# Performance work log

Hardware: AMD Instinct MI355X
Metric: run time of the kernel (lower is better)

## Reference

```python
import jax, jax.numpy as jnp
import numpy as np

# Sizes: batch=32, in_channels=32, out_channels=64, grid 256x256, modes1=modes2=32
B, CI, CO, NX, NY, M1, M2 = 32, 32, 64, 256, 256, 32, 32


def setup_inputs() -> dict:
    key = jax.random.key(0)
    k1, k2, k3 = jax.random.split(key, 3)
    scale = 1.0 / (CI * CO)
    return {
        "x": jax.random.normal(k1, (B, CI, NX, NY), dtype=jnp.float32),
        "w_real": scale * jax.random.uniform(k2, (CI, CO, 2 * M1, M2 + 1), dtype=jnp.float32),
        "w_imag": scale * jax.random.uniform(k3, (CI, CO, 2 * M1, M2 + 1), dtype=jnp.float32),
        "modes1": M1,
        "modes2": M2,
    }


def reference(x, w_real, w_imag, modes1, modes2):
    # rfft2 with 'forward' normalization (divide by nx*ny), as in torch.fft.rfft2(norm='forward')
    xf = jnp.fft.rfft2(x, norm="forward")  # (b, i, nx, ny//2+1) complex64
    # resize_rfft2(xf, (2*modes1, 2*modes2)) in the truncation regime (nx >= 2*m1, ny//2+1 >= m2+1):
    # keep first modes2+1 columns (rfft axis) and the first/last modes1 rows (full fft axis).
    xt = jnp.concatenate(
        [xf[..., :modes1, : modes2 + 1], xf[..., -modes1:, : modes2 + 1]], axis=-2
    )  # (b, i, 2*m1, m2+1)
    W = w_real + 1j * w_imag  # (i, o, 2*m1, m2+1) complex
    # complex channel mixing, keep only real part
    y = jnp.einsum("bixy,ioxy->boxy", xt, W).real  # (b, o, 2*m1, m2+1)
    # signed mode-sum: double-count conjugate-symmetric modes, correct the (0,0) DC mode
    out = (
        2.0 * jnp.sum(y[..., :modes1, :], axis=(-2, -1))
        + 2.0 * jnp.sum(y[..., modes1:, 1:], axis=(-2, -1))
        - y[..., 0, 0]
    )  # (b, o)
    return out
```

## Files before the change

kernel.cpp:

```cpp
#include <hip/hip_runtime.h>
#include <math.h>

#define BATCH 32
#define CIn   32
#define COut  64

typedef __attribute__((ext_vector_type(8))) short bf16x8;
typedef __attribute__((ext_vector_type(4))) float f32x4;

#define OB_T1F  0u
#define OB_ECF  40960u
#define OB_ESF  73728u
#define OB_XTB  106496u
#define OB_PART 8757248u

__device__ __forceinline__ ushort f2bf(float f) {
    union { float f; uint u; } v; v.f = f;
    uint r = (v.u + 0x7FFFu + ((v.u >> 16) & 1u)) >> 16;
    return (ushort)r;
}

__device__ __forceinline__ bf16x8 cvt8(f32x4 lo, f32x4 hi) {
    bf16x8 r;
    r[0] = (short)f2bf(lo[0]); r[1] = (short)f2bf(lo[1]);
    r[2] = (short)f2bf(lo[2]); r[3] = (short)f2bf(lo[3]);
    r[4] = (short)f2bf(hi[0]); r[5] = (short)f2bf(hi[1]);
    r[6] = (short)f2bf(hi[2]); r[7] = (short)f2bf(hi[3]);
    return r;
}

#define NB0 0
#define NB1 16
#define NB2 32
#define NB3 48
#define NB4 50

__global__ void fno_tw(ushort* __restrict__ T1f, ushort* __restrict__ Ecf,
                       ushort* __restrict__ Esf) {
    const int nb[5] = {NB0, NB1, NB2, NB3, NB4};
    int idx = blockIdx.x * 256 + threadIdx.x;
    const float w0 = 6.28318530717958647692f / 256.0f;
    if (idx < 20480) {
        int i = idx & 7, l = (idx >> 3) & 63, ct = idx >> 9;
        int c = ct / 5, t = ct - 5 * c;
        int k = 32 * c + 8 * (l >> 4) + i;
        int n = nb[t] + (l & 15);
        int ky = n >> 1, s = n & 1;
        int m = (k * ky) & 255;
        float v = s ? -sinf(w0 * (float)m) : cosf(w0 * (float)m);
        T1f[idx] = f2bf(v * (1.0f / 65536.0f));
    }
    if (idx < 16384) {
        int i = idx & 7, l = (idx >> 3) & 63, km = idx >> 9;
        int ks = km >> 2, mt = km & 3;
        int xx = ks * 32 + ((l >> 4) << 3) + i;
        int kx = mt * 16 + (l & 15);
        int kxa = (kx < 32) ? kx : kx + 192;
        int m = (xx * kxa) & 255;
        Ecf[idx] = f2bf(cosf(w0 * (float)m));
        Esf[idx] = f2bf(-sinf(w0 * (float)m));
    }
}

#define MFMA5(CG, AV)                                                              \
    acc0 = __builtin_amdgcn_mfma_f32_16x16x32_bf16((AV), bfr[(CG)*5+0], acc0, 0,0,0); \
    acc1 = __builtin_amdgcn_mfma_f32_16x16x32_bf16((AV), bfr[(CG)*5+1], acc1, 0,0,0); \
    acc2 = __builtin_amdgcn_mfma_f32_16x16x32_bf16((AV), bfr[(CG)*5+2], acc2, 0,0,0); \
    acc3 = __builtin_amdgcn_mfma_f32_16x16x32_bf16((AV), bfr[(CG)*5+3], acc3, 0,0,0); \
    acc4 = __builtin_amdgcn_mfma_f32_16x16x32_bf16((AV), bfr[(CG)*5+4], acc4, 0,0,0);

#define STAGE_CG(CG) do {                                                          \
    int cg_ = (CG);                                                                \
    const float* base_ = x + ((size_t)p * 256 + (size_t)(cg_ >> 2) * 64) * 256     \
                           + (cg_ & 3) * 64;                                       \
    float* buf_ = &smx[cg_ & 1][0];                                                \
    _Pragma("unroll")                                                              \
    for (int j = 0; j < 4; ++j) {                                                  \
        int rr_ = ((w * 4 + j) << 2) + (lane >> 4);                                \
        int sg_ = (lane & 15) ^ (rr_ & 7);                                         \
        const float* gp_ = base_ + (size_t)rr_ * 256 + (sg_ << 2);                 \
        char* lp_ = (char*)buf_ + ((w * 4 + j) << 10);                             \
        __builtin_amdgcn_global_load_lds(                                          \
            (const __attribute__((address_space(1))) unsigned int*)gp_,            \
            (__attribute__((address_space(3))) unsigned int*)lp_, 16, 0, 0);       \
    } } while (0)

#define WAITV(N) do {                                                              \
    asm volatile("s_waitcnt vmcnt(" #N ")" ::: "memory");                          \
    __builtin_amdgcn_sched_barrier(0); } while (0)

#define WAITL0 do {                                                                \
    asm volatile("s_waitcnt lgkmcnt(0)" ::: "memory");                             \
    __builtin_amdgcn_sched_barrier(0); } while (0)

#define YTW(ACC, T) do {                                                           \
    int n_ = nb[T] + r0;                                                           \
    if ((T) != 4 || r0 >= 14) {                                                    \
        _Pragma("unroll")                                                          \
        for (int j = 0; j < 4; ++j) {                                              \
            int xrow_ = sl * 64 + w * 16 + 4 * g + j;                              \
            int us_ = n_ * 256 + ((((xrow_ >> 3) ^ (n_ & 31)) << 3) | (xrow_ & 7));\
            Yt[us_] = f2bf((ACC)[j]);                                              \
        } } } while (0)

__global__ __launch_bounds__(256, 2)
void fno_fused(const float* __restrict__ x, const ushort* __restrict__ T1f,
               const ushort* __restrict__ Ecf, const ushort* __restrict__ Esf,
               ushort* __restrict__ XTb) {
    __shared__ float smx[2][4096];
    __shared__ __align__(16) ushort Yt[16896];
    const int nb[5] = {NB0, NB1, NB2, NB3, NB4};
    const int tid  = threadIdx.x;
    const int lane = tid & 63;
    const int w    = tid >> 6;
    const int r0   = lane & 15;
    const int g    = lane >> 4;
    const int p    = blockIdx.x;

    bf16x8 bfr[40];
    const bf16x8* bp = (const bf16x8*)T1f;
#pragma unroll
    for (int q = 0; q < 40; ++q) bfr[q] = bp[q * 64 + lane];

    const int rr = (w << 4) + r0;
    const int xr = rr & 7;

    STAGE_CG(0);
    STAGE_CG(1);

    f32x4 acc0, acc1, acc2, acc3, acc4;
#pragma unroll
    for (int cg = 0; cg < 16; ++cg) {
        if ((cg & 3) == 0) {
            acc0 = (f32x4){0,0,0,0}; acc1 = (f32x4){0,0,0,0};
            acc2 = (f32x4){0,0,0,0}; acc3 = (f32x4){0,0,0,0};
            acc4 = (f32x4){0,0,0,0};
        }
        if (cg < 15) { WAITV(4); } else { WAITV(0); }

        const float* rowp = &smx[cg & 1][rr * 64];
        f32x4 lo0 = *(const f32x4*)&rowp[(((g << 1)    ) ^ xr) << 2];
        f32x4 hi0 = *(const f32x4*)&rowp[(((g << 1) + 1) ^ xr) << 2];
        f32x4 lo1 = *(const f32x4*)&rowp[((8 + (g << 1)    ) ^ xr) << 2];
        f32x4 hi1 = *(const f32x4*)&rowp[((8 + (g << 1) + 1) ^ xr) << 2];
        WAITL0;
        if (cg + 2 < 16) STAGE_CG(cg + 2);

        bf16x8 a0v = cvt8(lo0, hi0);
        bf16x8 a1v = cvt8(lo1, hi1);
        MFMA5(2 * (cg & 3)    , a0v);
        MFMA5(2 * (cg & 3) + 1, a1v);

        if ((cg & 3) == 3) {
            int sl = cg >> 2;
            YTW(acc0, 0); YTW(acc1, 1); YTW(acc2, 2); YTW(acc3, 3); YTW(acc4, 4);
        }
    }
    __syncthreads();

    const int mt = w;
    f32x4 P1[5], P2[5];
#pragma unroll
    for (int t = 0; t < 5; ++t) { P1[t] = (f32x4){0,0,0,0}; P2[t] = (f32x4){0,0,0,0}; }

    const bf16x8* ecp = (const bf16x8*)Ecf;
    const bf16x8* esp = (const bf16x8*)Esf;
#pragma unroll
    for (int ks = 0; ks < 8; ++ks) {
        bf16x8 ea = ecp[(ks * 4 + mt) * 64 + lane];
        bf16x8 es = esp[(ks * 4 + mt) * 64 + lane];
#pragma unroll
        for (int t = 0; t < 5; ++t) {
            int n = nb[t] + r0;
            bf16x8 b = *(const bf16x8*)&Yt[n * 256 + ((((ks << 2) + g) ^ (n & 31)) << 3)];
            P1[t] = __builtin_amdgcn_mfma_f32_16x16x32_bf16(ea, b, P1[t], 0, 0, 0);
            P2[t] = __builtin_amdgcn_mfma_f32_16x16x32_bf16(es, b, P2[t], 0, 0, 0);
        }
    }

    ushort* xtl = (ushort*)&smx[0][0];
#pragma unroll
    for (int t = 0; t < 5; ++t) {
        int n  = nb[t] + r0;
        int ky = n >> 1, im = n & 1;
#pragma unroll
        for (int j = 0; j < 4; ++j) {
            float v2x = __shfl_xor(P2[t][j], 1);
            if (t == 4 && r0 < 14) continue;
            int kx = mt * 16 + 4 * g + j;
            float val = im ? (P1[t][j] + v2x) : (P1[t][j] - v2x);
            float wgt = (kx < 32) ? ((kx == 0 && ky == 0) ? 1.f : 2.f)
                                  : ((ky == 0) ? 0.f : 2.f);
            if (im) wgt = -wgt;
            xtl[kx * 66 + n] = f2bf(wgt * val);
        }
    }
    __syncthreads();

    const uint4* srcq = (const uint4*)xtl;
    uint4* dstq = (uint4*)(XTb + (size_t)p * 4224);
    for (int e = tid; e < 528; e += 256) dstq[e] = srcq[e];
}

__global__ __launch_bounds__(256)
void fno_gemm3(const ushort* __restrict__ XTb, const float* __restrict__ Wr,
               const float* __restrict__ Wi, float* __restrict__ part) {
    const int blk = blockIdx.x;
    const int ic  = blk / 22;
    const int sc  = blk - ic * 22;
    const int tid = threadIdx.x;
    const int lane = tid & 63;
    const int w    = tid >> 6;
    const int r0   = lane & 15;
    const int g    = lane >> 4;
    const int o    = (w << 4) + r0;

    const float* wrp = Wr + ((size_t)ic * 64 + o) * 2112 + sc * 96 + 4 * g;
    const float* wip = Wi + ((size_t)ic * 64 + o) * 2112 + sc * 96 + 4 * g;
    const ushort* a0 = XTb + ((size_t)r0 * 32 + ic) * 4224 + sc * 192 + 8 * g;
    const ushort* a1 = a0 + (size_t)16 * 32 * 4224;

    f32x4 acc0 = {0,0,0,0}, acc1 = {0,0,0,0};
#pragma unroll
    for (int st = 0; st < 6; ++st) {
        f32x4 vr = *(const f32x4*)(wrp + st * 16);
        f32x4 vi = *(const f32x4*)(wip + st * 16);
        bf16x8 b;
        b[0] = (short)f2bf(vr[0]); b[1] = (short)f2bf(vi[0]);
        b[2] = (short)f2bf(vr[1]); b[3] = (short)f2bf(vi[1]);
        b[4] = (short)f2bf(vr[2]); b[5] = (short)f2bf(vi[2]);
        b[6] = (short)f2bf(vr[3]); b[7] = (short)f2bf(vi[3]);
        bf16x8 af0 = *(const bf16x8*)(a0 + st * 32);
        bf16x8 af1 = *(const bf16x8*)(a1 + st * 32);
        acc0 = __builtin_amdgcn_mfma_f32_16x16x32_bf16(af0, b, acc0, 0, 0, 0);
        acc1 = __builtin_amdgcn_mfma_f32_16x16x32_bf16(af1, b, acc1, 0, 0, 0);
    }

    float* pp = part + (size_t)blk * 2048;
#pragma unroll
    for (int j = 0; j < 4; ++j) {
        pp[(4 * g + j) * 64 + o]      = acc0[j];
        pp[(16 + 4 * g + j) * 64 + o] = acc1[j];
    }
}

__global__ __launch_bounds__(256)
void fno_reduce(const float* __restrict__ part, float* __restrict__ out) {
    __shared__ float red[8][32];
    const int tid = threadIdx.x;
    const int il  = tid & 31;
    const int js  = tid >> 5;
    const int idx = blockIdx.x * 32 + il;

    float s = 0.f;
#pragma unroll 4
    for (int t = 0; t < 88; ++t)
        s += part[(size_t)(js + 8 * t) * 2048 + idx];
    red[js][il] = s;
    __syncthreads();

    if (tid < 32) {
        float v = red[0][tid] + red[1][tid] + red[2][tid] + red[3][tid]
                + red[4][tid] + red[5][tid] + red[6][tid] + red[7][tid];
        out[blockIdx.x * 32 + tid] = v;
    }
}

extern "C" void kernel_launch(void* const* d_in, const int* in_sizes, int n_in,
                              void* d_out, int out_size, void* d_ws, size_t ws_size,
                              hipStream_t stream) {
    const float* x  = (const float*)d_in[0];
    const float* wr = (const float*)d_in[1];
    const float* wi = (const float*)d_in[2];
    float* out = (float*)d_out;
    char* ws   = (char*)d_ws;

    ushort* T1f = (ushort*)(ws + OB_T1F);
    ushort* Ecf = (ushort*)(ws + OB_ECF);
    ushort* Esf = (ushort*)(ws + OB_ESF);
    ushort* XTb = (ushort*)(ws + OB_XTB);
    float* part = (float*)(ws + OB_PART);

    fno_tw<<<80, 256, 0, stream>>>(T1f, Ecf, Esf);
    fno_fused<<<1024, 256, 0, stream>>>(x, T1f, Ecf, Esf, XTb);
    fno_gemm3<<<704, 256, 0, stream>>>(XTb, wr, wi, part);
    fno_reduce<<<64, 256, 0, stream>>>(part, out);
}
```

Before: 85.03 us.

## Deepen x staging pipeline, use packed bf16 conversion, widen reduce grid

The fused DFT kernel now stages x in smaller 32-column chunks through a four-deep LDS ring, with three loads in flight. It prefetches the next chunk's LDS reads into registers before issuing the current MFMAs, so global latency and LDS reads overlap with matrix work. Scalar float-to-bf16 rounding is replaced with the HIP packed __float22bfloat162_rn conversions across all kernels, which cuts ALU work. The final reduction runs on 256 blocks instead of 64 to raise parallelism. The cost is more vmcnt bookkeeping and more loop iterations, each with smaller per-iteration work.

```diff
diff --git a/kernel.cpp b/kernel.cpp
--- a/kernel.cpp
+++ b/kernel.cpp
@@ -1,4 +1,5 @@
 #include <hip/hip_runtime.h>
+#include <hip/hip_bf16.h>
 #include <math.h>
 
 #define BATCH 32
@@ -20,13 +21,18 @@
     return (ushort)r;
 }
 
+__device__ __forceinline__ ushort f2bfn(float f) {
+    union { __hip_bfloat16 h; ushort u; } v;
+    v.h = __float2bfloat16(f);
+    return v.u;
+}
 __device__ __forceinline__ bf16x8 cvt8(f32x4 lo, f32x4 hi) {
-    bf16x8 r;
-    r[0] = (short)f2bf(lo[0]); r[1] = (short)f2bf(lo[1]);
-    r[2] = (short)f2bf(lo[2]); r[3] = (short)f2bf(lo[3]);
-    r[4] = (short)f2bf(hi[0]); r[5] = (short)f2bf(hi[1]);
-    r[6] = (short)f2bf(hi[2]); r[7] = (short)f2bf(hi[3]);
-    return r;
+    union { __hip_bfloat162 h2[4]; bf16x8 v; } u;
+    u.h2[0] = __float22bfloat162_rn(make_float2(lo[0], lo[1]));
+    u.h2[1] = __float22bfloat162_rn(make_float2(lo[2], lo[3]));
+    u.h2[2] = __float22bfloat162_rn(make_float2(hi[0], hi[1]));
+    u.h2[3] = __float22bfloat162_rn(make_float2(hi[2], hi[3]));
+    return u.v;
 }
 
 #define NB0 0
@@ -62,28 +68,33 @@
     }
 }
 
-#define MFMA5(CG, AV)                                                              \
-    acc0 = __builtin_amdgcn_mfma_f32_16x16x32_bf16((AV), bfr[(CG)*5+0], acc0, 0,0,0); \
-    acc1 = __builtin_amdgcn_mfma_f32_16x16x32_bf16((AV), bfr[(CG)*5+1], acc1, 0,0,0); \
-    acc2 = __builtin_amdgcn_mfma_f32_16x16x32_bf16((AV), bfr[(CG)*5+2], acc2, 0,0,0); \
-    acc3 = __builtin_amdgcn_mfma_f32_16x16x32_bf16((AV), bfr[(CG)*5+3], acc3, 0,0,0); \
-    acc4 = __builtin_amdgcn_mfma_f32_16x16x32_bf16((AV), bfr[(CG)*5+4], acc4, 0,0,0);
+#define MFMA5(KC, AV)                                                              \
+    acc0 = __builtin_amdgcn_mfma_f32_16x16x32_bf16((AV), bfr[(KC)*5+0], acc0, 0,0,0); \
+    acc1 = __builtin_amdgcn_mfma_f32_16x16x32_bf16((AV), bfr[(KC)*5+1], acc1, 0,0,0); \
+    acc2 = __builtin_amdgcn_mfma_f32_16x16x32_bf16((AV), bfr[(KC)*5+2], acc2, 0,0,0); \
+    acc3 = __builtin_amdgcn_mfma_f32_16x16x32_bf16((AV), bfr[(KC)*5+3], acc3, 0,0,0); \
+    acc4 = __builtin_amdgcn_mfma_f32_16x16x32_bf16((AV), bfr[(KC)*5+4], acc4, 0,0,0);
 
 #define STAGE_CG(CG) do {                                                          \
     int cg_ = (CG);                                                                \
-    const float* base_ = x + ((size_t)p * 256 + (size_t)(cg_ >> 2) * 64) * 256     \
-                           + (cg_ & 3) * 64;                                       \
-    float* buf_ = &smx[cg_ & 1][0];                                                \
+    int sl_ = cg_ >> 3, kc_ = cg_ & 7;                                             \
     _Pragma("unroll")                                                              \
-    for (int j = 0; j < 4; ++j) {                                                  \
-        int rr_ = ((w * 4 + j) << 2) + (lane >> 4);                                \
-        int sg_ = (lane & 15) ^ (rr_ & 7);                                         \
-        const float* gp_ = base_ + (size_t)rr_ * 256 + (sg_ << 2);                 \
-        char* lp_ = (char*)buf_ + ((w * 4 + j) << 10);                             \
+    for (int j = 0; j < 2; ++j) {                                                  \
+        int rws_ = 8 * j + (lane >> 3);                                            \
+        int sg_  = (lane & 7) ^ (rws_ & 7);                                        \
+        const float* gp_ = x + ((size_t)p * 256 + sl_ * 64 + w * 16 + rws_) * 256  \
+                             + kc_ * 32 + (sg_ << 2);                              \
+        char* lp_ = (char*)&smx[cg_ & 3][0] + w * 2048 + j * 1024 + (lane << 4);   \
         __builtin_amdgcn_global_load_lds(                                          \
             (const __attribute__((address_space(1))) unsigned int*)gp_,            \
             (__attribute__((address_space(3))) unsigned int*)lp_, 16, 0, 0);       \
     } } while (0)
+
+#define DSR(CG, RA, RB) do {                                                       \
+    const char* base_ = (const char*)&smx[(CG) & 3][0] + w * 2048 + r0 * 128;      \
+    (RA) = *(const f32x4*)(base_ + ((((g << 1)    ) ^ xr) << 4));                  \
+    (RB) = *(const f32x4*)(base_ + ((((g << 1) + 1) ^ xr) << 4));                  \
+    } while (0)
 
 #define WAITV(N) do {                                                              \
     asm volatile("s_waitcnt vmcnt(" #N ")" ::: "memory");                          \
@@ -100,14 +111,14 @@
         for (int j = 0; j < 4; ++j) {                                              \
             int xrow_ = sl * 64 + w * 16 + 4 * g + j;                              \
             int us_ = n_ * 256 + ((((xrow_ >> 3) ^ (n_ & 31)) << 3) | (xrow_ & 7));\
-            Yt[us_] = f2bf((ACC)[j]);                                              \
+            Yt[us_] = f2bfn((ACC)[j]);                                             \
         } } } while (0)
 
 __global__ __launch_bounds__(256, 2)
 void fno_fused(const float* __restrict__ x, const ushort* __restrict__ T1f,
                const ushort* __restrict__ Ecf, const ushort* __restrict__ Esf,
                ushort* __restrict__ XTb) {
-    __shared__ float smx[2][4096];
+    __shared__ float smx[4][2048];
     __shared__ __align__(16) ushort Yt[16896];
     const int nb[5] = {NB0, NB1, NB2, NB3, NB4};
     const int tid  = threadIdx.x;
@@ -115,6 +126,7 @@
     const int w    = tid >> 6;
     const int r0   = lane & 15;
     const int g    = lane >> 4;
+    const int xr   = r0 & 7;
     const int p    = blockIdx.x;
 
     bf16x8 bfr[40];
@@ -122,37 +134,30 @@
 #pragma unroll
     for (int q = 0; q < 40; ++q) bfr[q] = bp[q * 64 + lane];
 
-    const int rr = (w << 4) + r0;
-    const int xr = rr & 7;
-
-    STAGE_CG(0);
-    STAGE_CG(1);
+    f32x4 rA[2][2];
+
+    STAGE_CG(0); STAGE_CG(1); STAGE_CG(2);
+    WAITV(4);
+    DSR(0, rA[0][0], rA[0][1]);
 
     f32x4 acc0, acc1, acc2, acc3, acc4;
 #pragma unroll
-    for (int cg = 0; cg < 16; ++cg) {
-        if ((cg & 3) == 0) {
+    for (int cg = 0; cg < 32; ++cg) {
+        if ((cg & 7) == 0) {
             acc0 = (f32x4){0,0,0,0}; acc1 = (f32x4){0,0,0,0};
             acc2 = (f32x4){0,0,0,0}; acc3 = (f32x4){0,0,0,0};
             acc4 = (f32x4){0,0,0,0};
         }
-        if (cg < 15) { WAITV(4); } else { WAITV(0); }
-
-        const float* rowp = &smx[cg & 1][rr * 64];
-        f32x4 lo0 = *(const f32x4*)&rowp[(((g << 1)    ) ^ xr) << 2];
-        f32x4 hi0 = *(const f32x4*)&rowp[(((g << 1) + 1) ^ xr) << 2];
-        f32x4 lo1 = *(const f32x4*)&rowp[((8 + (g << 1)    ) ^ xr) << 2];
-        f32x4 hi1 = *(const f32x4*)&rowp[((8 + (g << 1) + 1) ^ xr) << 2];
         WAITL0;
-        if (cg + 2 < 16) STAGE_CG(cg + 2);
-
-        bf16x8 a0v = cvt8(lo0, hi0);
-        bf16x8 a1v = cvt8(lo1, hi1);
-        MFMA5(2 * (cg & 3)    , a0v);
-        MFMA5(2 * (cg & 3) + 1, a1v);
-
-        if ((cg & 3) == 3) {
-            int sl = cg >> 2;
+        bf16x8 af = cvt8(rA[cg & 1][0], rA[cg & 1][1]);
+        if (cg + 3 < 32) STAGE_CG(cg + 3);
+        if (cg <= 28)      { WAITV(4); }
+        else if (cg == 29) { WAITV(2); }
+        else if (cg == 30) { WAITV(0); }
+        if (cg + 1 < 32) DSR(cg + 1, rA[(cg + 1) & 1][0], rA[(cg + 1) & 1][1]);
+        MFMA5(cg & 7, af);
+        if ((cg & 7) == 7) {
+            int sl = cg >> 3;
             YTW(acc0, 0); YTW(acc1, 1); YTW(acc2, 2); YTW(acc3, 3); YTW(acc4, 4);
         }
     }
@@ -192,7 +197,7 @@
             float wgt = (kx < 32) ? ((kx == 0 && ky == 0) ? 1.f : 2.f)
                                   : ((ky == 0) ? 0.f : 2.f);
             if (im) wgt = -wgt;
-            xtl[kx * 66 + n] = f2bf(wgt * val);
+            xtl[kx * 66 + n] = f2bfn(wgt * val);
         }
     }
     __syncthreads();
@@ -225,15 +230,15 @@
     for (int st = 0; st < 6; ++st) {
         f32x4 vr = *(const f32x4*)(wrp + st * 16);
         f32x4 vi = *(const f32x4*)(wip + st * 16);
-        bf16x8 b;
-        b[0] = (short)f2bf(vr[0]); b[1] = (short)f2bf(vi[0]);
-        b[2] = (short)f2bf(vr[1]); b[3] = (short)f2bf(vi[1]);
-        b[4] = (short)f2bf(vr[2]); b[5] = (short)f2bf(vi[2]);
-        b[6] = (short)f2bf(vr[3]); b[7] = (short)f2bf(vi[3]);
+        union { __hip_bfloat162 h2[4]; bf16x8 v; } ub;
+        ub.h2[0] = __float22bfloat162_rn(make_float2(vr[0], vi[0]));
+        ub.h2[1] = __float22bfloat162_rn(make_float2(vr[1], vi[1]));
+        ub.h2[2] = __float22bfloat162_rn(make_float2(vr[2], vi[2]));
+        ub.h2[3] = __float22bfloat162_rn(make_float2(vr[3], vi[3]));
         bf16x8 af0 = *(const bf16x8*)(a0 + st * 32);
         bf16x8 af1 = *(const bf16x8*)(a1 + st * 32);
-        acc0 = __builtin_amdgcn_mfma_f32_16x16x32_bf16(af0, b, acc0, 0, 0, 0);
-        acc1 = __builtin_amdgcn_mfma_f32_16x16x32_bf16(af1, b, acc1, 0, 0, 0);
+        acc0 = __builtin_amdgcn_mfma_f32_16x16x32_bf16(af0, ub.v, acc0, 0, 0, 0);
+        acc1 = __builtin_amdgcn_mfma_f32_16x16x32_bf16(af1, ub.v, acc1, 0, 0, 0);
     }
 
     float* pp = part + (size_t)blk * 2048;
@@ -246,23 +251,24 @@
 
 __global__ __launch_bounds__(256)
 void fno_reduce(const float* __restrict__ part, float* __restrict__ out) {
-    __shared__ float red[8][32];
+    __shared__ float red[256];
     const int tid = threadIdx.x;
-    const int il  = tid & 31;
-    const int js  = tid >> 5;
-    const int idx = blockIdx.x * 32 + il;
+    const int il  = tid & 7;
+    const int js  = tid >> 3;
+    const int idx = blockIdx.x * 8 + il;
 
     float s = 0.f;
-#pragma unroll 4
-    for (int t = 0; t < 88; ++t)
-        s += part[(size_t)(js + 8 * t) * 2048 + idx];
-    red[js][il] = s;
+#pragma unroll
+    for (int t = 0; t < 22; ++t)
+        s += part[(size_t)(js + 32 * t) * 2048 + idx];
+    red[tid] = s;
     __syncthreads();
 
-    if (tid < 32) {
-        float v = red[0][tid] + red[1][tid] + red[2][tid] + red[3][tid]
-                + red[4][tid] + red[5][tid] + red[6][tid] + red[7][tid];
-        out[blockIdx.x * 32 + tid] = v;
+    if (tid < 8) {
+        float v = 0.f;
+#pragma unroll
+        for (int q = 0; q < 32; ++q) v += red[q * 8 + tid];
+        out[blockIdx.x * 8 + tid] = v;
     }
 }
 
@@ -284,5 +290,5 @@
     fno_tw<<<80, 256, 0, stream>>>(T1f, Ecf, Esf);
     fno_fused<<<1024, 256, 0, stream>>>(x, T1f, Ecf, Esf, XTb);
     fno_gemm3<<<704, 256, 0, stream>>>(XTb, wr, wi, part);
-    fno_reduce<<<64, 256, 0, stream>>>(part, out);
-}
+    fno_reduce<<<256, 256, 0, stream>>>(part, out);
+}
```

New measurement: 80.30 us. -5.6%, faster.
